# Optimization experiments

Hardware: AMD Instinct MI355X
Metric: run time of the kernel (lower is better)

## Reference

```python
import jax, jax.numpy as jnp
import numpy as np

B, T, D, F, E, K = 2, 1024, 1024, 2048, 8, 2

def setup_inputs() -> dict:
    key = jax.random.key(0)
    ks = jax.random.split(key, 9)
    s = 0.02
    return {
        "states": jax.random.normal(ks[0], (B, T, D), dtype=jnp.float32),
        "Wg": jax.random.normal(ks[1], (D, E), dtype=jnp.float32) * s,
        "W_in": jax.random.normal(ks[2], (E, D, F), dtype=jnp.float32) * s,
        "b_in": jnp.zeros((E, F), dtype=jnp.float32),
        "W_scale": jax.random.normal(ks[3], (E, D, F), dtype=jnp.float32) * s,
        "b_scale": jnp.zeros((E, F), dtype=jnp.float32),
        "W_out": jax.random.normal(ks[4], (E, F, D), dtype=jnp.float32) * s,
        "b_out": jnp.zeros((E, D), dtype=jnp.float32),
        "num_selected": K,
    }

def reference(states, Wg, W_in, b_in, W_scale, b_scale, W_out, b_out, num_selected):
    b, t, d = states.shape
    x = states.reshape(-1, d)                      # [N, D]
    n = x.shape[0]
    # router: softmax over experts, then top-k + renormalize
    probs = jax.nn.softmax(x @ Wg, axis=-1)        # [N, E]
    topw, topi = jax.lax.top_k(probs, num_selected)  # [N, K]
    topw = topw / topw.sum(axis=-1, keepdims=True)
    # dense combine weights [N, E]: zero except selected experts
    w_full = jnp.zeros_like(probs).at[jnp.arange(n)[:, None], topi].set(topw)
    # gated-GELU expert MLPs, batched over experts
    h = jnp.einsum('nd,edf->enf', x, W_in) + b_in[:, None, :]       # [E, N, F]
    s = jnp.einsum('nd,edf->enf', x, W_scale) + b_scale[:, None, :]
    inner = jax.nn.gelu(h, approximate=False) * s                    # exact GELU (torch default)
    y = jnp.einsum('enf,efd->end', inner, W_out) + b_out[:, None, :]  # [E, N, D]
    out = jnp.einsum('end,ne->nd', y, w_full)                         # weighted combine
    return out.reshape(b, t, d)
```

## Files before the change

### kernel.cpp

```cpp
#include <hip/hip_runtime.h>
#include <hip/hip_bf16.h>
#include <math.h>

#define N_TOK 2048
#define DIM   1024
#define FF    2048
#define NEXP  8
#define NSLOT (N_TOK * 2)

typedef __attribute__((ext_vector_type(8))) short short8;
typedef __attribute__((ext_vector_type(4))) float f32x4;
typedef _Float16 half_t;
typedef __attribute__((ext_vector_type(4))) _Float16 h16x4;

__device__ __forceinline__ unsigned short f2bf(float f) {
    unsigned int u = __float_as_uint(f);
    u += 0x7FFFu + ((u >> 16) & 1u);
    return (unsigned short)(u >> 16);
}

#define GLOAD_LDS16(g, l) \
    __builtin_amdgcn_global_load_lds((const __attribute__((address_space(1))) unsigned int*)(g), \
                                     (__attribute__((address_space(3))) unsigned int*)(l), 16, 0, 0)

__global__ __launch_bounds__(256) void k_router(const float* __restrict__ x,
        const float* __restrict__ Wg, int* __restrict__ hdr,
        int* __restrict__ tok_e, float* __restrict__ tok_w) {
    int wave = threadIdx.x >> 6, lane = threadIdx.x & 63;
    int t = blockIdx.x * 4 + wave;
    float acc[NEXP];
#pragma unroll
    for (int e = 0; e < NEXP; ++e) acc[e] = 0.f;
    const float* xr = x + (size_t)t * DIM;
    for (int d = lane; d < DIM; d += 64) {
        float xv = xr[d];
        const float* wr = Wg + d * NEXP;
#pragma unroll
        for (int e = 0; e < NEXP; ++e) acc[e] += xv * wr[e];
    }
#pragma unroll
    for (int off = 32; off > 0; off >>= 1) {
#pragma unroll
        for (int e = 0; e < NEXP; ++e) acc[e] += __shfl_down(acc[e], off);
    }
    if (lane == 0) {
        int e0 = 0;
#pragma unroll
        for (int e = 1; e < NEXP; ++e) if (acc[e] > acc[e0]) e0 = e;
        int e1 = -1;
#pragma unroll
        for (int e = 0; e < NEXP; ++e) {
            if (e == e0) continue;
            if (e1 < 0 || acc[e] > acc[e1]) e1 = e;
        }
        float w0 = 1.f / (1.f + expf(acc[e1] - acc[e0]));
        tok_e[2 * t] = e0; tok_e[2 * t + 1] = e1;
        tok_w[2 * t] = w0; tok_w[2 * t + 1] = 1.f - w0;
        atomicAdd(&hdr[e0], 1);
        atomicAdd(&hdr[e1], 1);
    }
}

__global__ void k_scan(int* hdr) {
    if (threadIdx.x == 0 && blockIdx.x == 0) {
        int s = 0;
        for (int e = 0; e < NEXP; ++e) {
            hdr[16 + e] = s;
            hdr[8 + e]  = s;
            s += hdr[e];
        }
        hdr[24] = s;
    }
}

__global__ __launch_bounds__(256) void k_assign(const float* __restrict__ x,
        int* __restrict__ hdr, const int* __restrict__ tok_e,
        int* __restrict__ tok_slot, unsigned short* __restrict__ xg) {
    __shared__ int sh[2];
    int t = blockIdx.x;
    if (threadIdx.x == 0) {
        int e0 = tok_e[2 * t], e1 = tok_e[2 * t + 1];
        int p0 = atomicAdd(&hdr[8 + e0], 1);
        int p1 = atomicAdd(&hdr[8 + e1], 1);
        tok_slot[2 * t] = p0; tok_slot[2 * t + 1] = p1;
        sh[0] = p0; sh[1] = p1;
    }
    __syncthreads();
    int s0 = sh[0], s1 = sh[1];
    const float4* xr = (const float4*)(x + (size_t)t * DIM);
    float4 v = xr[threadIdx.x];
    ushort4 b;
    b.x = f2bf(v.x); b.y = f2bf(v.y); b.z = f2bf(v.z); b.w = f2bf(v.w);
    ((ushort4*)(xg + (size_t)s0 * DIM))[threadIdx.x] = b;
    ((ushort4*)(xg + (size_t)s1 * DIM))[threadIdx.x] = b;
}

__global__ __launch_bounds__(256) void k_cvt(
        const float* __restrict__ s0, const float* __restrict__ s1,
        const float* __restrict__ s2, unsigned short* __restrict__ d0,
        unsigned short* __restrict__ d1, unsigned short* __restrict__ d2) {
    int bz = blockIdx.y;
    int which = bz >> 3, e = bz & 7;
    int R = (which == 2) ? FF : DIM;
    int C = (which == 2) ? DIM : FF;
    const float* S = ((which == 0) ? s0 : (which == 1) ? s1 : s2) + (size_t)e * DIM * FF;
    unsigned short* D = ((which == 0) ? d0 : (which == 1) ? d1 : d2) + (size_t)e * DIM * FF;
    int tilesx = C >> 6;
    int tx = blockIdx.x % tilesx, ty = blockIdx.x / tilesx;
    int c0 = tx * 64, r0 = ty * 64;
    __shared__ unsigned short sh[64][65];
    int t = threadIdx.x;
    int rr = t >> 4, cc = (t & 15) * 4;
#pragma unroll
    for (int j = 0; j < 4; ++j) {
        int r = rr + j * 16;
        float4 v = *(const float4*)(S + (size_t)(r0 + r) * C + c0 + cc);
        sh[r][cc + 0] = f2bf(v.x);
        sh[r][cc + 1] = f2bf(v.y);
        sh[r][cc + 2] = f2bf(v.z);
        sh[r][cc + 3] = f2bf(v.w);
    }
    __syncthreads();
    int oc = t >> 2, orr = (t & 3) * 16;
    unsigned short tmp[16];
#pragma unroll
    for (int j = 0; j < 16; ++j) tmp[j] = sh[orr + j][oc];
    unsigned short* q = D + (size_t)(c0 + oc) * R + r0 + orr;
    *(uint4*)q       = *(uint4*)&tmp[0];
    *(uint4*)(q + 8) = *(uint4*)&tmp[8];
}

__global__ __launch_bounds__(256, 2) void k_expert_hs(
        const unsigned short* __restrict__ xg,
        const unsigned short* __restrict__ Wth,
        const unsigned short* __restrict__ Wts,
        const float* __restrict__ b_in, const float* __restrict__ b_sc,
        const int* __restrict__ hdr, unsigned short* __restrict__ inner) {
    int e = blockIdx.z;
    int cnt = hdr[e];
    int mtile = blockIdx.y;
    if (mtile * 128 >= cnt) return;
    int base = hdr[16 + e];
    int f0 = blockIdx.x * 128;

    __shared__ unsigned short As[2 * 128 * 32];
    __shared__ unsigned short Bh[2 * 128 * 32];
    __shared__ unsigned short Bs[2 * 128 * 32];

    int tid = threadIdx.x;
    int wave = tid >> 6, lane = tid & 63;
    int lr = lane & 15, lq = lane >> 4;
    int wm = (wave >> 1) * 64, wf = (wave & 1) * 64;

    f32x4 acch[4][4], accs[4][4];
#pragma unroll
    for (int mi = 0; mi < 4; ++mi)
#pragma unroll
        for (int fi = 0; fi < 4; ++fi) {
            acch[mi][fi] = (f32x4){0.f, 0.f, 0.f, 0.f};
            accs[mi][fi] = (f32x4){0.f, 0.f, 0.f, 0.f};
        }

    int swzc = (lane & 3) ^ ((lane >> 3) & 3);
    int goff = (lane >> 2) * DIM + swzc * 8;
    int rdo = lr * 32 + (lq ^ ((lr >> 1) & 3)) * 8;

    const unsigned short* Abase = xg  + (size_t)(base + mtile * 128) * DIM + goff;
    const unsigned short* Hbase = Wth + ((size_t)e * FF + f0) * DIM + goff;
    const unsigned short* Sbase = Wts + ((size_t)e * FF + f0) * DIM + goff;
    int p0 = wave * 32, p1 = wave * 32 + 16;

    GLOAD_LDS16(Abase + (size_t)p0 * DIM, &As[p0 * 32]);
    GLOAD_LDS16(Abase + (size_t)p1 * DIM, &As[p1 * 32]);
    GLOAD_LDS16(Hbase + (size_t)p0 * DIM, &Bh[p0 * 32]);
    GLOAD_LDS16(Hbase + (size_t)p1 * DIM, &Bh[p1 * 32]);
    GLOAD_LDS16(Sbase + (size_t)p0 * DIM, &Bs[p0 * 32]);
    GLOAD_LDS16(Sbase + (size_t)p1 * DIM, &Bs[p1 * 32]);
    __syncthreads();

    const int NSTEP = DIM / 32;
    for (int t = 0; t < NSTEP; ++t) {
        int co = (t & 1) * (128 * 32);
        if (t + 1 < NSTEP) {
            int no = ((t & 1) ^ 1) * (128 * 32);
            int k1 = (t + 1) * 32;
            GLOAD_LDS16(Abase + (size_t)p0 * DIM + k1, &As[no + p0 * 32]);
            GLOAD_LDS16(Abase + (size_t)p1 * DIM + k1, &As[no + p1 * 32]);
            GLOAD_LDS16(Hbase + (size_t)p0 * DIM + k1, &Bh[no + p0 * 32]);
            GLOAD_LDS16(Hbase + (size_t)p1 * DIM + k1, &Bh[no + p1 * 32]);
            GLOAD_LDS16(Sbase + (size_t)p0 * DIM + k1, &Bs[no + p0 * 32]);
            GLOAD_LDS16(Sbase + (size_t)p1 * DIM + k1, &Bs[no + p1 * 32]);
        }

        short8 af[4], bhf[4], bsf[4];
#pragma unroll
        for (int mi = 0; mi < 4; ++mi)
            af[mi] = *(const short8*)&As[co + (wm + mi * 16) * 32 + rdo];
#pragma unroll
        for (int fi = 0; fi < 4; ++fi) {
            bhf[fi] = *(const short8*)&Bh[co + (wf + fi * 16) * 32 + rdo];
            bsf[fi] = *(const short8*)&Bs[co + (wf + fi * 16) * 32 + rdo];
        }
#pragma unroll
        for (int mi = 0; mi < 4; ++mi)
#pragma unroll
            for (int fi = 0; fi < 4; ++fi) {
                acch[mi][fi] = __builtin_amdgcn_mfma_f32_16x16x32_bf16(
                    af[mi], bhf[fi], acch[mi][fi], 0, 0, 0);
                accs[mi][fi] = __builtin_amdgcn_mfma_f32_16x16x32_bf16(
                    af[mi], bsf[fi], accs[mi][fi], 0, 0, 0);
            }
        __syncthreads();
    }

#pragma unroll
    for (int fi = 0; fi < 4; ++fi) {
        int f = f0 + wf + fi * 16 + lr;
        float bi = b_in[e * FF + f];
        float bs2 = b_sc[e * FF + f];
#pragma unroll
        for (int mi = 0; mi < 4; ++mi) {
#pragma unroll
            for (int r = 0; r < 4; ++r) {
                int rl = wm + mi * 16 + lq * 4 + r;
                int grow = mtile * 128 + rl;
                if (grow < cnt) {
                    float h = acch[mi][fi][r] + bi;
                    float s = accs[mi][fi][r] + bs2;
                    float g = 0.5f * h * (1.f + erff(h * 0.70710678f));
                    inner[(size_t)(base + grow) * FF + f] = f2bf(g * s);
                }
            }
        }
    }
}

__global__ __launch_bounds__(256, 2) void k_expert_out(
        const unsigned short* __restrict__ inner,
        const unsigned short* __restrict__ Wto,
        const int* __restrict__ hdr, half_t* __restrict__ pbuf) {
    int e = blockIdx.z & 7;
    int ks = blockIdx.z >> 3;
    int cnt = hdr[e];
    int mtile = blockIdx.y;
    if (mtile * 128 >= cnt) return;
    int base = hdr[16 + e];
    int d0 = blockIdx.x * 256;

    __shared__ unsigned short As[2 * 128 * 32];
    __shared__ unsigned short Bt[2 * 256 * 32];

    int tid = threadIdx.x;
    int wave = tid >> 6, lane = tid & 63;
    int lr = lane & 15, lq = lane >> 4;
    int wm = (wave >> 1) * 64, wn = (wave & 1) * 128;

    f32x4 acc[4][8];
#pragma unroll
    for (int mi = 0; mi < 4; ++mi)
#pragma unroll
        for (int ni = 0; ni < 8; ++ni) acc[mi][ni] = (f32x4){0.f, 0.f, 0.f, 0.f};

    int swzc = (lane & 3) ^ ((lane >> 3) & 3);
    int goff = (lane >> 2) * FF + swzc * 8;
    int rdo = lr * 32 + (lq ^ ((lr >> 1) & 3)) * 8;

    const unsigned short* Abase = inner + (size_t)(base + mtile * 128) * FF + goff;
    const unsigned short* Bbase = Wto + ((size_t)e * DIM + d0) * FF + goff;
    int pa0 = wave * 32, pa1 = wave * 32 + 16;
    int pb0 = wave * 64;

    int kbeg = ks * (FF / 2);

    GLOAD_LDS16(Abase + (size_t)pa0 * FF + kbeg, &As[pa0 * 32]);
    GLOAD_LDS16(Abase + (size_t)pa1 * FF + kbeg, &As[pa1 * 32]);
#pragma unroll
    for (int j = 0; j < 4; ++j)
        GLOAD_LDS16(Bbase + (size_t)(pb0 + j * 16) * FF + kbeg, &Bt[(pb0 + j * 16) * 32]);
    __syncthreads();

    const int NSTEP = (FF / 2) / 32;
    for (int t = 0; t < NSTEP; ++t) {
        int coA = (t & 1) * (128 * 32), coB = (t & 1) * (256 * 32);
        if (t + 1 < NSTEP) {
            int noA = ((t & 1) ^ 1) * (128 * 32), noB = ((t & 1) ^ 1) * (256 * 32);
            int k1 = kbeg + (t + 1) * 32;
            GLOAD_LDS16(Abase + (size_t)pa0 * FF + k1, &As[noA + pa0 * 32]);
            GLOAD_LDS16(Abase + (size_t)pa1 * FF + k1, &As[noA + pa1 * 32]);
#pragma unroll
            for (int j = 0; j < 4; ++j)
                GLOAD_LDS16(Bbase + (size_t)(pb0 + j * 16) * FF + k1, &Bt[noB + (pb0 + j * 16) * 32]);
        }

        short8 af[4], bfm[8];
#pragma unroll
        for (int mi = 0; mi < 4; ++mi)
            af[mi] = *(const short8*)&As[coA + (wm + mi * 16) * 32 + rdo];
#pragma unroll
        for (int ni = 0; ni < 8; ++ni)
            bfm[ni] = *(const short8*)&Bt[coB + (wn + ni * 16) * 32 + rdo];
#pragma unroll
        for (int mi = 0; mi < 4; ++mi)
#pragma unroll
            for (int ni = 0; ni < 8; ++ni)
                acc[mi][ni] = __builtin_amdgcn_mfma_f32_16x16x32_bf16(
                    af[mi], bfm[ni], acc[mi][ni], 0, 0, 0);
        __syncthreads();
    }

    half_t* P = pbuf + (size_t)ks * NSLOT * DIM;
#pragma unroll
    for (int ni = 0; ni < 8; ++ni) {
        int d = d0 + wn + ni * 16 + lr;
#pragma unroll
        for (int mi = 0; mi < 4; ++mi) {
#pragma unroll
            for (int r = 0; r < 4; ++r) {
                int rl = wm + mi * 16 + lq * 4 + r;
                int grow = mtile * 128 + rl;
                if (grow < cnt)
                    P[(size_t)(base + grow) * DIM + d] = (half_t)acc[mi][ni][r];
            }
        }
    }
}

__global__ __launch_bounds__(256) void k_combine(const half_t* __restrict__ pbuf,
        const int* __restrict__ tok_slot, const int* __restrict__ tok_e,
        const float* __restrict__ tok_w, const float* __restrict__ b_out,
        float* __restrict__ out) {
    int t = blockIdx.x;
    int d = threadIdx.x * 4;
    int s0 = tok_slot[2 * t], s1 = tok_slot[2 * t + 1];
    int e0 = tok_e[2 * t], e1 = tok_e[2 * t + 1];
    float w0 = tok_w[2 * t], w1 = tok_w[2 * t + 1];
    const half_t* pA = pbuf;
    const half_t* pB = pbuf + (size_t)NSLOT * DIM;
    h16x4 a0 = *(const h16x4*)&pA[(size_t)s0 * DIM + d];
    h16x4 a1 = *(const h16x4*)&pB[(size_t)s0 * DIM + d];
    h16x4 c0 = *(const h16x4*)&pA[(size_t)s1 * DIM + d];
    h16x4 c1 = *(const h16x4*)&pB[(size_t)s1 * DIM + d];
    float4 b0 = *(const float4*)&b_out[e0 * DIM + d];
    float4 b1 = *(const float4*)&b_out[e1 * DIM + d];
    float4 r;
    r.x = w0 * ((float)a0.x + (float)a1.x + b0.x) + w1 * ((float)c0.x + (float)c1.x + b1.x);
    r.y = w0 * ((float)a0.y + (float)a1.y + b0.y) + w1 * ((float)c0.y + (float)c1.y + b1.y);
    r.z = w0 * ((float)a0.z + (float)a1.z + b0.z) + w1 * ((float)c0.z + (float)c1.z + b1.z);
    r.w = w0 * ((float)a0.w + (float)a1.w + b0.w) + w1 * ((float)c0.w + (float)c1.w + b1.w);
    *(float4*)&out[(size_t)t * DIM + d] = r;
}

extern "C" void kernel_launch(void* const* d_in, const int* in_sizes, int n_in,
                              void* d_out, int out_size, void* d_ws, size_t ws_size,
                              hipStream_t stream) {
    (void)in_sizes; (void)n_in; (void)out_size; (void)ws_size;
    const float* x    = (const float*)d_in[0];
    const float* Wg   = (const float*)d_in[1];
    const float* Win  = (const float*)d_in[2];
    const float* b_in = (const float*)d_in[3];
    const float* Wsc  = (const float*)d_in[4];
    const float* b_sc = (const float*)d_in[5];
    const float* Wout = (const float*)d_in[6];
    const float* b_out= (const float*)d_in[7];
    float* out = (float*)d_out;

    char* ws = (char*)d_ws;
    int*   hdr      = (int*)ws;
    int*   tok_e    = (int*)(ws + 256);
    float* tok_w    = (float*)(ws + 16640);
    int*   tok_slot = (int*)(ws + 33024);
    unsigned short* xg    = (unsigned short*)(ws + 65792);
    unsigned short* inner = (unsigned short*)(ws + 65792 + 8388608);
    half_t* pbuf = (half_t*)(ws + 65792 + 8388608 + 16777216);
    unsigned short* wt_h = (unsigned short*)(ws + 65792 + 8388608 + 16777216 + 16777216);
    unsigned short* wt_s = wt_h + (size_t)NEXP * FF * DIM;
    unsigned short* wt_o = wt_s + (size_t)NEXP * FF * DIM;

    hipMemsetAsync(hdr, 0, 256, stream);
    k_cvt<<<dim3(512, 24), dim3(256), 0, stream>>>(Win, Wsc, Wout, wt_h, wt_s, wt_o);
    k_router<<<dim3(N_TOK / 4), dim3(256), 0, stream>>>(x, Wg, hdr, tok_e, tok_w);
    k_scan<<<dim3(1), dim3(64), 0, stream>>>(hdr);
    k_assign<<<dim3(N_TOK), dim3(256), 0, stream>>>(x, hdr, tok_e, tok_slot, xg);
    k_expert_hs<<<dim3(FF / 128, 16, NEXP), dim3(256), 0, stream>>>(xg, wt_h, wt_s, b_in, b_sc, hdr, inner);
    k_expert_out<<<dim3(DIM / 256, 16, NEXP * 2), dim3(256), 0, stream>>>(inner, wt_o, hdr, pbuf);
    k_combine<<<dim3(N_TOK), dim3(256), 0, stream>>>(pbuf, tok_slot, tok_e, tok_w, b_out, out);
}
```

Baseline: 470.1 us.

## Shrink expert GEMM tiles for higher occupancy and rework weight transpose kernel

The gate/scale GEMM F-tile drops from 128 to 64 and the output GEMM D-tile from 256 to 128. Both raise launch bounds to 4 blocks per CU, cutting accumulator registers and LDS per block so more waves can hide latency and more blocks can launch. The weight conversion kernel now handles 128-row tiles, writes transposed into shared memory and emits 16-byte row stores. The cost is less reuse of each A tile per block and more redundant activation loads, plus possible LDS bank conflicts in the new transpose write pattern.

```diff
diff --git a/kernel.cpp b/kernel.cpp
--- a/kernel.cpp
+++ b/kernel.cpp
@@ -107,30 +107,32 @@
     unsigned short* D = ((which == 0) ? d0 : (which == 1) ? d1 : d2) + (size_t)e * DIM * FF;
     int tilesx = C >> 6;
     int tx = blockIdx.x % tilesx, ty = blockIdx.x / tilesx;
-    int c0 = tx * 64, r0 = ty * 64;
-    __shared__ unsigned short sh[64][65];
+    int c0 = tx * 64, r0 = ty * 128;
+    __shared__ unsigned short sh[64][132];
     int t = threadIdx.x;
-    int rr = t >> 4, cc = (t & 15) * 4;
-#pragma unroll
-    for (int j = 0; j < 4; ++j) {
-        int r = rr + j * 16;
-        float4 v = *(const float4*)(S + (size_t)(r0 + r) * C + c0 + cc);
-        sh[r][cc + 0] = f2bf(v.x);
-        sh[r][cc + 1] = f2bf(v.y);
-        sh[r][cc + 2] = f2bf(v.z);
-        sh[r][cc + 3] = f2bf(v.w);
+    int rl = t >> 4, cl = (t & 15) * 4;
+#pragma unroll
+    for (int p = 0; p < 8; ++p) {
+        int r = p * 16 + rl;
+        float4 v = *(const float4*)(S + (size_t)(r0 + r) * C + c0 + cl);
+        sh[cl + 0][r] = f2bf(v.x);
+        sh[cl + 1][r] = f2bf(v.y);
+        sh[cl + 2][r] = f2bf(v.z);
+        sh[cl + 3][r] = f2bf(v.w);
     }
     __syncthreads();
-    int oc = t >> 2, orr = (t & 3) * 16;
-    unsigned short tmp[16];
-#pragma unroll
-    for (int j = 0; j < 16; ++j) tmp[j] = sh[orr + j][oc];
-    unsigned short* q = D + (size_t)(c0 + oc) * R + r0 + orr;
-    *(uint4*)q       = *(uint4*)&tmp[0];
-    *(uint4*)(q + 8) = *(uint4*)&tmp[8];
-}
-
-__global__ __launch_bounds__(256, 2) void k_expert_hs(
+    int ol = t >> 4, wl = (t & 15) * 8;
+#pragma unroll
+    for (int p = 0; p < 4; ++p) {
+        int oc = p * 16 + ol;
+        uint2 lo = *(const uint2*)&sh[oc][wl];
+        uint2 hi = *(const uint2*)&sh[oc][wl + 4];
+        uint4 v = make_uint4(lo.x, lo.y, hi.x, hi.y);
+        *(uint4*)(D + (size_t)(c0 + oc) * R + r0 + wl) = v;
+    }
+}
+
+__global__ __launch_bounds__(256, 4) void k_expert_hs(
         const unsigned short* __restrict__ xg,
         const unsigned short* __restrict__ Wth,
         const unsigned short* __restrict__ Wts,
@@ -141,22 +143,22 @@
     int mtile = blockIdx.y;
     if (mtile * 128 >= cnt) return;
     int base = hdr[16 + e];
-    int f0 = blockIdx.x * 128;
+    int f0 = blockIdx.x * 64;
 
     __shared__ unsigned short As[2 * 128 * 32];
-    __shared__ unsigned short Bh[2 * 128 * 32];
-    __shared__ unsigned short Bs[2 * 128 * 32];
+    __shared__ unsigned short Bh[2 * 64 * 32];
+    __shared__ unsigned short Bs[2 * 64 * 32];
 
     int tid = threadIdx.x;
     int wave = tid >> 6, lane = tid & 63;
     int lr = lane & 15, lq = lane >> 4;
-    int wm = (wave >> 1) * 64, wf = (wave & 1) * 64;
-
-    f32x4 acch[4][4], accs[4][4];
+    int wm = (wave >> 1) * 64, wf = (wave & 1) * 32;
+
+    f32x4 acch[4][2], accs[4][2];
 #pragma unroll
     for (int mi = 0; mi < 4; ++mi)
 #pragma unroll
-        for (int fi = 0; fi < 4; ++fi) {
+        for (int fi = 0; fi < 2; ++fi) {
             acch[mi][fi] = (f32x4){0.f, 0.f, 0.f, 0.f};
             accs[mi][fi] = (f32x4){0.f, 0.f, 0.f, 0.f};
         }
@@ -168,43 +170,39 @@
     const unsigned short* Abase = xg  + (size_t)(base + mtile * 128) * DIM + goff;
     const unsigned short* Hbase = Wth + ((size_t)e * FF + f0) * DIM + goff;
     const unsigned short* Sbase = Wts + ((size_t)e * FF + f0) * DIM + goff;
-    int p0 = wave * 32, p1 = wave * 32 + 16;
-
-    GLOAD_LDS16(Abase + (size_t)p0 * DIM, &As[p0 * 32]);
-    GLOAD_LDS16(Abase + (size_t)p1 * DIM, &As[p1 * 32]);
-    GLOAD_LDS16(Hbase + (size_t)p0 * DIM, &Bh[p0 * 32]);
-    GLOAD_LDS16(Hbase + (size_t)p1 * DIM, &Bh[p1 * 32]);
-    GLOAD_LDS16(Sbase + (size_t)p0 * DIM, &Bs[p0 * 32]);
-    GLOAD_LDS16(Sbase + (size_t)p1 * DIM, &Bs[p1 * 32]);
+    int pa0 = wave * 16, pa1 = 64 + wave * 16, pb = wave * 16;
+
+    GLOAD_LDS16(Abase + (size_t)pa0 * DIM, &As[pa0 * 32]);
+    GLOAD_LDS16(Abase + (size_t)pa1 * DIM, &As[pa1 * 32]);
+    GLOAD_LDS16(Hbase + (size_t)pb * DIM, &Bh[pb * 32]);
+    GLOAD_LDS16(Sbase + (size_t)pb * DIM, &Bs[pb * 32]);
     __syncthreads();
 
     const int NSTEP = DIM / 32;
     for (int t = 0; t < NSTEP; ++t) {
-        int co = (t & 1) * (128 * 32);
+        int coA = (t & 1) * (128 * 32), coB = (t & 1) * (64 * 32);
         if (t + 1 < NSTEP) {
-            int no = ((t & 1) ^ 1) * (128 * 32);
+            int noA = ((t & 1) ^ 1) * (128 * 32), noB = ((t & 1) ^ 1) * (64 * 32);
             int k1 = (t + 1) * 32;
-            GLOAD_LDS16(Abase + (size_t)p0 * DIM + k1, &As[no + p0 * 32]);
-            GLOAD_LDS16(Abase + (size_t)p1 * DIM + k1, &As[no + p1 * 32]);
-            GLOAD_LDS16(Hbase + (size_t)p0 * DIM + k1, &Bh[no + p0 * 32]);
-            GLOAD_LDS16(Hbase + (size_t)p1 * DIM + k1, &Bh[no + p1 * 32]);
-            GLOAD_LDS16(Sbase + (size_t)p0 * DIM + k1, &Bs[no + p0 * 32]);
-            GLOAD_LDS16(Sbase + (size_t)p1 * DIM + k1, &Bs[no + p1 * 32]);
-        }
-
-        short8 af[4], bhf[4], bsf[4];
+            GLOAD_LDS16(Abase + (size_t)pa0 * DIM + k1, &As[noA + pa0 * 32]);
+            GLOAD_LDS16(Abase + (size_t)pa1 * DIM + k1, &As[noA + pa1 * 32]);
+            GLOAD_LDS16(Hbase + (size_t)pb * DIM + k1, &Bh[noB + pb * 32]);
+            GLOAD_LDS16(Sbase + (size_t)pb * DIM + k1, &Bs[noB + pb * 32]);
+        }
+
+        short8 af[4], bhf[2], bsf[2];
 #pragma unroll
         for (int mi = 0; mi < 4; ++mi)
-            af[mi] = *(const short8*)&As[co + (wm + mi * 16) * 32 + rdo];
-#pragma unroll
-        for (int fi = 0; fi < 4; ++fi) {
-            bhf[fi] = *(const short8*)&Bh[co + (wf + fi * 16) * 32 + rdo];
-            bsf[fi] = *(const short8*)&Bs[co + (wf + fi * 16) * 32 + rdo];
+            af[mi] = *(const short8*)&As[coA + (wm + mi * 16) * 32 + rdo];
+#pragma unroll
+        for (int fi = 0; fi < 2; ++fi) {
+            bhf[fi] = *(const short8*)&Bh[coB + (wf + fi * 16) * 32 + rdo];
+            bsf[fi] = *(const short8*)&Bs[coB + (wf + fi * 16) * 32 + rdo];
         }
 #pragma unroll
         for (int mi = 0; mi < 4; ++mi)
 #pragma unroll
-            for (int fi = 0; fi < 4; ++fi) {
+            for (int fi = 0; fi < 2; ++fi) {
                 acch[mi][fi] = __builtin_amdgcn_mfma_f32_16x16x32_bf16(
                     af[mi], bhf[fi], acch[mi][fi], 0, 0, 0);
                 accs[mi][fi] = __builtin_amdgcn_mfma_f32_16x16x32_bf16(
@@ -214,7 +212,7 @@
     }
 
 #pragma unroll
-    for (int fi = 0; fi < 4; ++fi) {
+    for (int fi = 0; fi < 2; ++fi) {
         int f = f0 + wf + fi * 16 + lr;
         float bi = b_in[e * FF + f];
         float bs2 = b_sc[e * FF + f];
@@ -235,7 +233,7 @@
     }
 }
 
-__global__ __launch_bounds__(256, 2) void k_expert_out(
+__global__ __launch_bounds__(256, 4) void k_expert_out(
         const unsigned short* __restrict__ inner,
         const unsigned short* __restrict__ Wto,
         const int* __restrict__ hdr, half_t* __restrict__ pbuf) {
@@ -245,21 +243,21 @@
     int mtile = blockIdx.y;
     if (mtile * 128 >= cnt) return;
     int base = hdr[16 + e];
-    int d0 = blockIdx.x * 256;
+    int d0 = blockIdx.x * 128;
 
     __shared__ unsigned short As[2 * 128 * 32];
-    __shared__ unsigned short Bt[2 * 256 * 32];
+    __shared__ unsigned short Bt[2 * 128 * 32];
 
     int tid = threadIdx.x;
     int wave = tid >> 6, lane = tid & 63;
     int lr = lane & 15, lq = lane >> 4;
-    int wm = (wave >> 1) * 64, wn = (wave & 1) * 128;
-
-    f32x4 acc[4][8];
+    int wm = (wave >> 1) * 64, wn = (wave & 1) * 64;
+
+    f32x4 acc[4][4];
 #pragma unroll
     for (int mi = 0; mi < 4; ++mi)
 #pragma unroll
-        for (int ni = 0; ni < 8; ++ni) acc[mi][ni] = (f32x4){0.f, 0.f, 0.f, 0.f};
+        for (int ni = 0; ni < 4; ++ni) acc[mi][ni] = (f32x4){0.f, 0.f, 0.f, 0.f};
 
     int swzc = (lane & 3) ^ ((lane >> 3) & 3);
     int goff = (lane >> 2) * FF + swzc * 8;
@@ -267,42 +265,39 @@
 
     const unsigned short* Abase = inner + (size_t)(base + mtile * 128) * FF + goff;
     const unsigned short* Bbase = Wto + ((size_t)e * DIM + d0) * FF + goff;
-    int pa0 = wave * 32, pa1 = wave * 32 + 16;
-    int pb0 = wave * 64;
+    int pa0 = wave * 16, pa1 = 64 + wave * 16;
 
     int kbeg = ks * (FF / 2);
 
     GLOAD_LDS16(Abase + (size_t)pa0 * FF + kbeg, &As[pa0 * 32]);
     GLOAD_LDS16(Abase + (size_t)pa1 * FF + kbeg, &As[pa1 * 32]);
-#pragma unroll
-    for (int j = 0; j < 4; ++j)
-        GLOAD_LDS16(Bbase + (size_t)(pb0 + j * 16) * FF + kbeg, &Bt[(pb0 + j * 16) * 32]);
+    GLOAD_LDS16(Bbase + (size_t)pa0 * FF + kbeg, &Bt[pa0 * 32]);
+    GLOAD_LDS16(Bbase + (size_t)pa1 * FF + kbeg, &Bt[pa1 * 32]);
     __syncthreads();
 
     const int NSTEP = (FF / 2) / 32;
     for (int t = 0; t < NSTEP; ++t) {
-        int coA = (t & 1) * (128 * 32), coB = (t & 1) * (256 * 32);
+        int co = (t & 1) * (128 * 32);
         if (t + 1 < NSTEP) {
-            int noA = ((t & 1) ^ 1) * (128 * 32), noB = ((t & 1) ^ 1) * (256 * 32);
+            int no = ((t & 1) ^ 1) * (128 * 32);
             int k1 = kbeg + (t + 1) * 32;
-            GLOAD_LDS16(Abase + (size_t)pa0 * FF + k1, &As[noA + pa0 * 32]);
-            GLOAD_LDS16(Abase + (size_t)pa1 * FF + k1, &As[noA + pa1 * 32]);
-#pragma unroll
-            for (int j = 0; j < 4; ++j)
-                GLOAD_LDS16(Bbase + (size_t)(pb0 + j * 16) * FF + k1, &Bt[noB + (pb0 + j * 16) * 32]);
-        }
-
-        short8 af[4], bfm[8];
+            GLOAD_LDS16(Abase + (size_t)pa0 * FF + k1, &As[no + pa0 * 32]);
+            GLOAD_LDS16(Abase + (size_t)pa1 * FF + k1, &As[no + pa1 * 32]);
+            GLOAD_LDS16(Bbase + (size_t)pa0 * FF + k1, &Bt[no + pa0 * 32]);
+            GLOAD_LDS16(Bbase + (size_t)pa1 * FF + k1, &Bt[no + pa1 * 32]);
+        }
+
+        short8 af[4], bfm[4];
 #pragma unroll
         for (int mi = 0; mi < 4; ++mi)
-            af[mi] = *(const short8*)&As[coA + (wm + mi * 16) * 32 + rdo];
-#pragma unroll
-        for (int ni = 0; ni < 8; ++ni)
-            bfm[ni] = *(const short8*)&Bt[coB + (wn + ni * 16) * 32 + rdo];
+            af[mi] = *(const short8*)&As[co + (wm + mi * 16) * 32 + rdo];
+#pragma unroll
+        for (int ni = 0; ni < 4; ++ni)
+            bfm[ni] = *(const short8*)&Bt[co + (wn + ni * 16) * 32 + rdo];
 #pragma unroll
         for (int mi = 0; mi < 4; ++mi)
 #pragma unroll
-            for (int ni = 0; ni < 8; ++ni)
+            for (int ni = 0; ni < 4; ++ni)
                 acc[mi][ni] = __builtin_amdgcn_mfma_f32_16x16x32_bf16(
                     af[mi], bfm[ni], acc[mi][ni], 0, 0, 0);
         __syncthreads();
@@ -310,7 +305,7 @@
 
     half_t* P = pbuf + (size_t)ks * NSLOT * DIM;
 #pragma unroll
-    for (int ni = 0; ni < 8; ++ni) {
+    for (int ni = 0; ni < 4; ++ni) {
         int d = d0 + wn + ni * 16 + lr;
 #pragma unroll
         for (int mi = 0; mi < 4; ++mi) {
@@ -377,11 +372,11 @@
     unsigned short* wt_o = wt_s + (size_t)NEXP * FF * DIM;
 
     hipMemsetAsync(hdr, 0, 256, stream);
-    k_cvt<<<dim3(512, 24), dim3(256), 0, stream>>>(Win, Wsc, Wout, wt_h, wt_s, wt_o);
+    k_cvt<<<dim3(256, 24), dim3(256), 0, stream>>>(Win, Wsc, Wout, wt_h, wt_s, wt_o);
     k_router<<<dim3(N_TOK / 4), dim3(256), 0, stream>>>(x, Wg, hdr, tok_e, tok_w);
     k_scan<<<dim3(1), dim3(64), 0, stream>>>(hdr);
     k_assign<<<dim3(N_TOK), dim3(256), 0, stream>>>(x, hdr, tok_e, tok_slot, xg);
-    k_expert_hs<<<dim3(FF / 128, 16, NEXP), dim3(256), 0, stream>>>(xg, wt_h, wt_s, b_in, b_sc, hdr, inner);
-    k_expert_out<<<dim3(DIM / 256, 16, NEXP * 2), dim3(256), 0, stream>>>(inner, wt_o, hdr, pbuf);
+    k_expert_hs<<<dim3(FF / 64, 16, NEXP), dim3(256), 0, stream>>>(xg, wt_h, wt_s, b_in, b_sc, hdr, inner);
+    k_expert_out<<<dim3(DIM / 128, 16, NEXP * 2), dim3(256), 0, stream>>>(inner, wt_o, hdr, pbuf);
     k_combine<<<dim3(N_TOK), dim3(256), 0, stream>>>(pbuf, tok_slot, tok_e, tok_w, b_out, out);
 }
```

After: 446.0 us. 1.05x faster.
